# Optimization experiments

Measured on AMD Instinct MI355X. Metric: run time of the kernel, lower is better.

## Reference

```python
import jax, jax.numpy as jnp
import numpy as np

N = 200000      # active voxels
CIN = 96        # in_channels == out_channels (identity residual path)
CMID = 192      # max(in,out) * channel_multiplier
OFF = 27        # kernel_size**3 offsets
EPS = 1e-5      # BatchNorm eps


def setup_inputs() -> dict:
    key = jax.random.key(0)
    ks = jax.random.split(key, 6)
    x = jax.random.normal(ks[0], (N, CIN), jnp.float32)
    idx = jax.random.randint(ks[1], (OFF, N), 0, N, jnp.int32)
    mask = jax.random.randint(ks[2], (OFF, N), 0, 2, jnp.int32)
    W1 = jax.random.normal(ks[3], (OFF, CIN, CMID), jnp.float32) / np.float32(np.sqrt(OFF * CIN))
    W2 = jax.random.normal(ks[4], (OFF, CMID, CIN), jnp.float32) / np.float32(np.sqrt(OFF * CMID))
    g1 = jnp.ones((CMID,), jnp.float32)
    b1 = jnp.zeros((CMID,), jnp.float32)
    g2 = jnp.ones((CIN,), jnp.float32)
    b2 = jnp.zeros((CIN,), jnp.float32)
    return {"x": x, "idx": idx, "mask": mask, "W1": W1, "g1": g1, "b1": b1,
            "W2": W2, "g2": g2, "b2": b2}


def _sparse_conv(x, idx, mask, W):
    """Explicit-GEMM sparse conv: per-offset gather -> GEMM -> accumulate.
    x: [N, Cin], idx/mask: [OFF, N], W: [OFF, Cin, Cout] -> [N, Cout]."""
    n = x.shape[0]
    cout = W.shape[-1]

    def body(acc, off):
        i, m, w = off
        g = jnp.where(m[:, None] > 0, x[i], jnp.zeros((), x.dtype))  # gather [N, Cin]
        return acc + g @ w, None

    out, _ = jax.lax.scan(body, jnp.zeros((n, cout), x.dtype), (idx, mask, W))
    return out


def _bn(x, gamma, beta):
    # BatchNorm1d in training mode: batch statistics over the voxel dim.
    mu = jnp.mean(x, axis=0)
    var = jnp.var(x, axis=0)
    return gamma * (x - mu) * jax.lax.rsqrt(var + EPS) + beta


def reference(x, idx, mask, W1, g1, b1, W2, g2, b2):
    h = jax.nn.relu(_bn(_sparse_conv(x, idx, mask, W1), g1, b1))
    h = _bn(_sparse_conv(h, idx, mask, W2), g2, b2)
    return jax.nn.relu(h + x)  # identity residual (in_channels == out_channels)
```

## Files before the change

### kernel.cpp

```cpp
#include <hip/hip_runtime.h>
#include <hip/hip_bf16.h>

typedef unsigned short u16;
typedef __attribute__((ext_vector_type(8))) short short8;
typedef __attribute__((ext_vector_type(4))) float f32x4;
typedef __attribute__((ext_vector_type(8))) unsigned short ushort8v;

#define NVOX 200000
#define NVP  200064
#define NOFF 27
#define NBLK 1563

__device__ __forceinline__ u16 f2bf(float f) {
    __hip_bfloat16 h = __float2bfloat16(f);
    return *reinterpret_cast<u16*>(&h);
}
__device__ __forceinline__ float bf2f(u16 u) {
    union { unsigned int i; float f; } v;
    v.i = ((unsigned int)u) << 16;
    return v.f;
}

#define GLOAD_LDS16(g, l)                                                     \
    __builtin_amdgcn_global_load_lds(                                         \
        (const __attribute__((address_space(1))) unsigned int*)(g),           \
        (__attribute__((address_space(3))) unsigned int*)(l), 16, 0, 0)

__device__ __forceinline__ uint4 gld128(const u16* p) {
    uint4 r;
    asm volatile("global_load_dwordx4 %0, %1, off" : "=v"(r) : "v"(p) : "memory");
    return r;
}
__device__ __forceinline__ int gld32(const int* p) {
    int r;
    asm volatile("global_load_dword %0, %1, off" : "=v"(r) : "v"(p) : "memory");
    return r;
}
__device__ __forceinline__ uint4 dsr128(const u16* p) {
    uint4 r;
    asm volatile("ds_read_b128 %0, %1"
                 : "=v"(r)
                 : "v"((const __attribute__((address_space(3))) uint4*)p));
    return r;
}
__device__ __forceinline__ short8 as_s8(uint4 v) {
    union { uint4 u; short8 s; } c; c.u = v; return c.s;
}
#define S_WAIT_VM(n) asm volatile("s_waitcnt vmcnt(" #n ")" ::: "memory")
#define S_WAIT_LG(n) asm volatile("s_waitcnt lgkmcnt(" #n ")" ::: "memory")
#define SBAR0()      __builtin_amdgcn_sched_barrier(0)

__global__ __launch_bounds__(256) void prep_kernel(
    const float* __restrict__ x, const float* __restrict__ W1,
    const float* __restrict__ W2, u16* __restrict__ xb,
    u16* __restrict__ w1t, u16* __restrict__ w2t, float* __restrict__ zbuf)
{
    const int XV = NVOX * 96 / 4;
    const int WC = 62208;
    int t = blockIdx.x * 256 + threadIdx.x;
    if (blockIdx.x == 0 && threadIdx.x < 64) zbuf[threadIdx.x] = 0.f;
    if (t < XV) {
        float4 v = *(const float4*)(x + (size_t)t * 4);
        ushort4 o;
        o.x = f2bf(v.x); o.y = f2bf(v.y); o.z = f2bf(v.z); o.w = f2bf(v.w);
        *(ushort4*)(xb + (size_t)t * 4) = o;
    } else if (t < XV + WC) {
        int j = t - XV;
        int lane = j & 63, rest = j >> 6;
        int nco = rest % 12, rest2 = rest / 12;
        int ks = rest2 % 3, off = rest2 / 3;
        int co = nco * 16 + (lane & 15);
        int kb = ks * 32 + (lane >> 4) * 8;
        const float* src = W1 + (size_t)off * 18432 + (size_t)kb * 192 + co;
        ushort8v ov;
#pragma unroll
        for (int jj = 0; jj < 8; ++jj) ov[jj] = f2bf(src[(size_t)jj * 192]);
        *(ushort8v*)(w1t + (size_t)j * 8) = ov;
    } else if (t < XV + 2 * WC) {
        int j = t - XV - WC;
        int lane = j & 63, rest = j >> 6;
        int nco = rest % 6, rest2 = rest / 6;
        int kk = rest2 % 6, off = rest2 / 6;
        int co = nco * 16 + (lane & 15);
        int kb = kk * 32 + (lane >> 4) * 8;
        const float* src = W2 + (size_t)off * 18432 + (size_t)kb * 96 + co;
        ushort8v ov;
#pragma unroll
        for (int jj = 0; jj < 8; ++jj) ov[jj] = f2bf(src[(size_t)jj * 96]);
        *(ushort8v*)(w2t + (size_t)j * 8) = ov;
    }
}

__global__ __launch_bounds__(256) void lsrc_kernel(
    const int* __restrict__ idxp, const int* __restrict__ mskp,
    int* __restrict__ lsrcG)
{
    int r = blockIdx.x * 256 + threadIdx.x;
    int o = blockIdx.y;
    if (r < NVP) {
        int v = -1;
        if (r < NVOX) {
            if (mskp[(size_t)o * NVOX + r] > 0) v = idxp[(size_t)o * NVOX + r];
        }
        lsrcG[(size_t)o * NVP + r] = v;
    }
}

template<int COUT, int WN, int HFDIV>
__global__ __launch_bounds__(512, 4) void conv_mfma(
    const u16* __restrict__ xb, const int* __restrict__ lsrcG,
    const u16* __restrict__ Wt, const float* __restrict__ zbuf,
    u16* __restrict__ hout, float* __restrict__ part)
{
    constexpr int CIN  = 96 * HFDIV;
    constexpr int WM   = 8 / WN;
    constexpr int FM   = 128 / (WM * 16);
    constexpr int FN   = COUT / (WN * 16);
    constexpr int NCO  = COUT / 16;
    constexpr int SG   = NOFF * HFDIV;
    constexpr int BUFU = 12288;
    constexpr int WSTP = 3 * NCO * 512;

    __shared__ u16 ldsA[3 * BUFU];

    const int tid  = threadIdx.x;
    const int row0 = blockIdx.x * 128;
    const int lane = tid & 63;
    const int wid  = tid >> 6;
    const int wm   = wid / WN;
    const int wn   = wid % WN;
    const int lr   = lane & 15;
    const int lk   = lane >> 4;

    const int rStage = wid * 16 + (lane & 15);
    const int cBase  = (lane >> 4) * 8;
    const int ldsWaveBase = wid * 512;

    int rdBase[FM];
#pragma unroll
    for (int m = 0; m < FM; ++m)
        rdBase[m] = (wm * FM + m) * 512 + lr * 8 + lk * 128;
    const u16* wtw = Wt + (size_t)(wn * FN) * 512 + (size_t)lane * 8;
    const int* lsp = lsrcG + row0 + rStage;

    f32x4 acc[FM][FN];
#pragma unroll
    for (int m = 0; m < FM; ++m)
#pragma unroll
        for (int n = 0; n < FN; ++n)
            acc[m][n] = (f32x4){0.f, 0.f, 0.f, 0.f};

    auto gatherTo = [&](int sv, int hf, int bsel) {
        const u16* g = (sv >= 0)
            ? (xb + (size_t)sv * CIN + hf * 96 + cBase)
            : ((const u16*)zbuf + cBase);
#pragma unroll
        for (int it = 0; it < 3; ++it)
            GLOAD_LDS16(g + it * 32,
                        ldsA + bsel * BUFU + it * 4096 + ldsWaveBase);
    };
    auto svAddr = [&](int s) -> const int* {
        int idx2 = (s < SG) ? s : (SG - 1);
        int offIdx = (HFDIV == 1) ? idx2 : (idx2 >> 1);
        return lsp + (size_t)offIdx * NVP;
    };

    uint4 wregU[3 * FN];
    auto loadW = [&](const u16* wb) {
#pragma unroll
        for (int ks = 0; ks < 3; ++ks)
#pragma unroll
            for (int n = 0; n < FN; ++n)
                wregU[ks * FN + n] = gld128(wb + (ks * NCO + n) * 512);
    };
    auto mfmaPhase = [&](int cur) {
        const u16* abuf = ldsA + cur * BUFU;
        uint4 a[FM], b[FM];
#pragma unroll
        for (int m = 0; m < FM; ++m) a[m] = dsr128(abuf + rdBase[m]);
#pragma unroll
        for (int m = 0; m < FM; ++m) b[m] = dsr128(abuf + 4096 + rdBase[m]);
        if constexpr (FM == 4) S_WAIT_LG(4); else S_WAIT_LG(2);
        SBAR0();
#pragma unroll
        for (int m = 0; m < FM; ++m)
#pragma unroll
            for (int n = 0; n < FN; ++n)
                acc[m][n] = __builtin_amdgcn_mfma_f32_16x16x32_bf16(
                    as_s8(a[m]), as_s8(wregU[n]), acc[m][n], 0, 0, 0);
#pragma unroll
        for (int m = 0; m < FM; ++m) a[m] = dsr128(abuf + 8192 + rdBase[m]);
        if constexpr (FM == 4) S_WAIT_LG(4); else S_WAIT_LG(2);
        SBAR0();
#pragma unroll
        for (int m = 0; m < FM; ++m)
#pragma unroll
            for (int n = 0; n < FN; ++n)
                acc[m][n] = __builtin_amdgcn_mfma_f32_16x16x32_bf16(
                    as_s8(b[m]), as_s8(wregU[FN + n]), acc[m][n], 0, 0, 0);
        S_WAIT_LG(0);
        SBAR0();
#pragma unroll
        for (int m = 0; m < FM; ++m)
#pragma unroll
            for (int n = 0; n < FN; ++n)
                acc[m][n] = __builtin_amdgcn_mfma_f32_16x16x32_bf16(
                    as_s8(a[m]), as_s8(wregU[2 * FN + n]), acc[m][n], 0, 0, 0);
    };

    int sv0 = gld32(svAddr(0));
    int sv1 = gld32(svAddr(1));
    S_WAIT_VM(0); SBAR0();
    gatherTo(sv0, 0, 0);
    gatherTo(sv1, (HFDIV == 1) ? 0 : 1, 1);
    int svPend = gld32(svAddr(2));
    S_WAIT_VM(4); SBAR0();
    __builtin_amdgcn_s_barrier();
    SBAR0();

    const u16* wb = wtw;
    int cur = 0, nxt2 = 2;
#pragma unroll 1
    for (int s = 0; s < SG - 2; ++s) {
        loadW(wb);  wb += WSTP;
        SBAR0();
        S_WAIT_VM(9); SBAR0();
        int sv = svPend;
        gatherTo(sv, (HFDIV == 1) ? 0 : ((s + 2) & 1), nxt2);
        svPend = gld32(svAddr(s + 3));
        SBAR0();
        S_WAIT_VM(4); SBAR0();
        mfmaPhase(cur);
        SBAR0();
        __builtin_amdgcn_s_barrier();
        SBAR0();
        cur  = (cur == 2)  ? 0 : cur + 1;
        nxt2 = (nxt2 == 2) ? 0 : nxt2 + 1;
    }
    loadW(wb);  wb += WSTP;
    SBAR0();
    S_WAIT_VM(0); SBAR0();
    mfmaPhase(cur);
    SBAR0();
    __builtin_amdgcn_s_barrier();
    SBAR0();
    cur = (cur == 2) ? 0 : cur + 1;
    loadW(wb);
    SBAR0();
    S_WAIT_VM(0); SBAR0();
    mfmaPhase(cur);

    __syncthreads();
    float* smf = (float*)ldsA;
#pragma unroll
    for (int n = 0; n < FN; ++n) {
        float s1 = 0.f, s2 = 0.f;
#pragma unroll
        for (int m = 0; m < FM; ++m)
#pragma unroll
            for (int q = 0; q < 4; ++q) {
                float v = acc[m][n][q];
                s1 += v; s2 += v * v;
            }
        s1 += __shfl_xor(s1, 16); s1 += __shfl_xor(s1, 32);
        s2 += __shfl_xor(s2, 16); s2 += __shfl_xor(s2, 32);
        if (lane < 16) {
            int col = wn * (FN * 16) + n * 16 + lr;
            smf[(wm * COUT + col) * 2 + 0] = s1;
            smf[(wm * COUT + col) * 2 + 1] = s2;
        }
    }
    __syncthreads();
    if (tid < 2 * COUT) {
        int z = tid / COUT, cc = tid % COUT;
        float v = 0.f;
#pragma unroll
        for (int w = 0; w < WM; ++w) v += smf[(w * COUT + cc) * 2 + z];
        part[(size_t)blockIdx.x * (2 * COUT) + z * COUT + cc] = v;
    }

#pragma unroll
    for (int m = 0; m < FM; ++m) {
#pragma unroll
        for (int q = 0; q < 4; ++q) {
            int row = row0 + wm * (FM * 16) + m * 16 + lk * 4 + q;
            if (row < NVOX) {
#pragma unroll
                for (int n = 0; n < FN; ++n) {
                    int col = wn * (FN * 16) + n * 16 + lr;
                    hout[(size_t)row * COUT + col] = f2bf(acc[m][n][q]);
                }
            }
        }
    }
}

template<int COUT>
__global__ __launch_bounds__(256) void bn_statsB(
    const float* __restrict__ part, const float* __restrict__ g,
    const float* __restrict__ bv, float* __restrict__ ss)
{
    const int c = blockIdx.x;
    const int t = threadIdx.x;
    float s1 = 0.f, s2 = 0.f;
    for (int b = t; b < NBLK; b += 256) {
        s1 += part[(size_t)b * 2 * COUT + c];
        s2 += part[(size_t)b * 2 * COUT + COUT + c];
    }
#pragma unroll
    for (int d = 1; d < 64; d <<= 1) {
        s1 += __shfl_xor(s1, d);
        s2 += __shfl_xor(s2, d);
    }
    __shared__ float rs[8];
    int w = t >> 6;
    if ((t & 63) == 0) { rs[w] = s1; rs[4 + w] = s2; }
    __syncthreads();
    if (t == 0) {
        s1 = rs[0] + rs[1] + rs[2] + rs[3];
        s2 = rs[4] + rs[5] + rs[6] + rs[7];
        float mu  = s1 * (1.0f / NVOX);
        float var = s2 * (1.0f / NVOX) - mu * mu;
        float sc  = g[c] * rsqrtf(var + 1e-5f);
        ss[c] = sc;
        ss[COUT + c] = bv[c] - mu * sc;
    }
}

template<int COUT>
__global__ __launch_bounds__(256) void bn_apply_relu(
    u16* __restrict__ h, const float* __restrict__ ss)
{
    int t = blockIdx.x * 256 + threadIdx.x;
    int c0 = (t * 8) % COUT;
    ushort8v v = *(ushort8v*)(h + (size_t)t * 8);
#pragma unroll
    for (int j = 0; j < 8; ++j) {
        float f = bf2f(v[j]);
        f = fmaxf(f * ss[c0 + j] + ss[COUT + c0 + j], 0.f);
        v[j] = f2bf(f);
    }
    *(ushort8v*)(h + (size_t)t * 8) = v;
}

__global__ __launch_bounds__(256) void final_kernel(
    const u16* __restrict__ h2, const float* __restrict__ x,
    const float* __restrict__ ss, float* __restrict__ out)
{
    int t = blockIdx.x * 256 + threadIdx.x;
    int c0 = (t * 8) % 96;
    ushort8v v = *(const ushort8v*)(h2 + (size_t)t * 8);
    float4 x0 = *(const float4*)(x + (size_t)t * 8);
    float4 x1 = *(const float4*)(x + (size_t)t * 8 + 4);
    float xs[8] = {x0.x, x0.y, x0.z, x0.w, x1.x, x1.y, x1.z, x1.w};
    float o[8];
#pragma unroll
    for (int j = 0; j < 8; ++j) {
        float f = bf2f(v[j]) * ss[c0 + j] + ss[96 + c0 + j] + xs[j];
        o[j] = fmaxf(f, 0.f);
    }
    *(float4*)(out + (size_t)t * 8)     = (float4){o[0], o[1], o[2], o[3]};
    *(float4*)(out + (size_t)t * 8 + 4) = (float4){o[4], o[5], o[6], o[7]};
}

extern "C" void kernel_launch(void* const* d_in, const int* in_sizes, int n_in,
                              void* d_out, int out_size, void* d_ws, size_t ws_size,
                              hipStream_t stream)
{
    const float* x    = (const float*)d_in[0];
    const int*   idx  = (const int*)d_in[1];
    const int*   mask = (const int*)d_in[2];
    const float* W1   = (const float*)d_in[3];
    const float* g1   = (const float*)d_in[4];
    const float* b1   = (const float*)d_in[5];
    const float* W2   = (const float*)d_in[6];
    const float* g2   = (const float*)d_in[7];
    const float* b2   = (const float*)d_in[8];

    unsigned char* ws = (unsigned char*)d_ws;
    u16*  xb    = (u16*)ws;
    u16*  w1t   = (u16*)(ws + 38400000);
    u16*  w2t   = (u16*)(ws + 39395328);
    u16*  h2    = (u16*)(ws + 40390656);
    float* part = (float*)(ws + 78790656);
    float* ss1  = (float*)(ws + 81191424);
    float* ss2  = (float*)(ws + 81192960);
    float* zbuf = (float*)(ws + 81193728);
    int*  lsrcG = (int*)(ws + 81193984);

    u16* h = (u16*)d_out;

    prep_kernel<<<19236, 256, 0, stream>>>(x, W1, W2, xb, w1t, w2t, zbuf);
    lsrc_kernel<<<dim3(782, 27), 256, 0, stream>>>(idx, mask, lsrcG);

    conv_mfma<192, 4, 1><<<NBLK, 512, 0, stream>>>(xb, lsrcG, w1t, zbuf, h, part);
    bn_statsB<192><<<192, 256, 0, stream>>>(part, g1, b1, ss1);
    bn_apply_relu<192><<<18750, 256, 0, stream>>>(h, ss1);

    conv_mfma<96, 2, 2><<<NBLK, 512, 0, stream>>>(h, lsrcG, w2t, zbuf, h2, part);
    bn_statsB<96><<<96, 256, 0, stream>>>(part, g2, b2, ss2);
    final_kernel<<<9375, 256, 0, stream>>>(h2, x, ss2, (float*)d_out);
}
```

Measured before the change: 703.5 us.

## Stage conv weights into double-buffered LDS via direct global-to-LDS loads

Each wave no longer loads its weight fragments from global memory into registers. The block now cooperatively stages each offset's weight slice into a double-buffered LDS region using global_load_lds, with the weights repacked and padded in prep so the copies are contiguous. MFMA phases then read weights with ds_read alongside the activation reads. The aim is to cut redundant global weight traffic, since every wave re-read the same slice, and to lower VGPR pressure. In exchange LDS use grows and launch bounds drop from 4 to 2 blocks per CU, which may reduce occupancy.

```diff
diff --git a/kernel.cpp b/kernel.cpp
--- a/kernel.cpp
+++ b/kernel.cpp
@@ -26,11 +26,6 @@
         (const __attribute__((address_space(1))) unsigned int*)(g),           \
         (__attribute__((address_space(3))) unsigned int*)(l), 16, 0, 0)
 
-__device__ __forceinline__ uint4 gld128(const u16* p) {
-    uint4 r;
-    asm volatile("global_load_dwordx4 %0, %1, off" : "=v"(r) : "v"(p) : "memory");
-    return r;
-}
 __device__ __forceinline__ int gld32(const int* p) {
     int r;
     asm volatile("global_load_dword %0, %1, off" : "=v"(r) : "v"(p) : "memory");
@@ -75,19 +70,21 @@
         ushort8v ov;
 #pragma unroll
         for (int jj = 0; jj < 8; ++jj) ov[jj] = f2bf(src[(size_t)jj * 192]);
-        *(ushort8v*)(w1t + (size_t)j * 8) = ov;
+        *(ushort8v*)(w1t + (size_t)off * 20480 + (ks * 12 + nco) * 512 + lane * 8) = ov;
     } else if (t < XV + 2 * WC) {
         int j = t - XV - WC;
         int lane = j & 63, rest = j >> 6;
         int nco = rest % 6, rest2 = rest / 6;
-        int kk = rest2 % 6, off = rest2 / 6;
+        int ks = rest2 % 3, rest3 = rest2 / 3;
+        int hf = rest3 % 2, off = rest3 / 2;
         int co = nco * 16 + (lane & 15);
-        int kb = kk * 32 + (lane >> 4) * 8;
+        int kb = hf * 96 + ks * 32 + (lane >> 4) * 8;
         const float* src = W2 + (size_t)off * 18432 + (size_t)kb * 96 + co;
         ushort8v ov;
 #pragma unroll
         for (int jj = 0; jj < 8; ++jj) ov[jj] = f2bf(src[(size_t)jj * 96]);
-        *(ushort8v*)(w2t + (size_t)j * 8) = ov;
+        *(ushort8v*)(w2t + (size_t)(off * 2 + hf) * 12288 +
+                     (ks * 6 + nco) * 512 + lane * 8) = ov;
     }
 }
 
@@ -107,7 +104,7 @@
 }
 
 template<int COUT, int WN, int HFDIV>
-__global__ __launch_bounds__(512, 4) void conv_mfma(
+__global__ __launch_bounds__(512, 2) void conv_mfma(
     const u16* __restrict__ xb, const int* __restrict__ lsrcG,
     const u16* __restrict__ Wt, const float* __restrict__ zbuf,
     u16* __restrict__ hout, float* __restrict__ part)
@@ -119,9 +116,12 @@
     constexpr int NCO  = COUT / 16;
     constexpr int SG   = NOFF * HFDIV;
     constexpr int BUFU = 12288;
-    constexpr int WSTP = 3 * NCO * 512;
+    constexpr int WPAD = (COUT == 192) ? 2560 : 1536;
+    constexpr int WCH  = WPAD / 512;
+    constexpr int WBUFU = WPAD * 8;
 
     __shared__ u16 ldsA[3 * BUFU];
+    __shared__ u16 ldsW[2 * WBUFU];
 
     const int tid  = threadIdx.x;
     const int row0 = blockIdx.x * 128;
@@ -135,12 +135,13 @@
     const int rStage = wid * 16 + (lane & 15);
     const int cBase  = (lane >> 4) * 8;
     const int ldsWaveBase = wid * 512;
+    const int wStageBase  = (tid & ~63) * 8;
 
     int rdBase[FM];
 #pragma unroll
     for (int m = 0; m < FM; ++m)
         rdBase[m] = (wm * FM + m) * 512 + lr * 8 + lk * 128;
-    const u16* wtw = Wt + (size_t)(wn * FN) * 512 + (size_t)lane * 8;
+    const int wfBase = (wn * FN) * 512 + lane * 8;
     const int* lsp = lsrcG + row0 + rStage;
 
     f32x4 acc[FM][FN];
@@ -150,54 +151,60 @@
         for (int n = 0; n < FN; ++n)
             acc[m][n] = (f32x4){0.f, 0.f, 0.f, 0.f};
 
-    auto gatherTo = [&](int sv, int hf, int bsel) {
-        const u16* g = (sv >= 0)
-            ? (xb + (size_t)sv * CIN + hf * 96 + cBase)
-            : ((const u16*)zbuf + cBase);
-#pragma unroll
-        for (int it = 0; it < 3; ++it)
-            GLOAD_LDS16(g + it * 32,
-                        ldsA + bsel * BUFU + it * 4096 + ldsWaveBase);
-    };
+    auto hfOf = [&](int s) -> int { return (HFDIV == 1) ? 0 : (s & 1); };
     auto svAddr = [&](int s) -> const int* {
         int idx2 = (s < SG) ? s : (SG - 1);
         int offIdx = (HFDIV == 1) ? idx2 : (idx2 >> 1);
         return lsp + (size_t)offIdx * NVP;
     };
-
-    uint4 wregU[3 * FN];
-    auto loadW = [&](const u16* wb) {
-#pragma unroll
-        for (int ks = 0; ks < 3; ++ks)
-#pragma unroll
-            for (int n = 0; n < FN; ++n)
-                wregU[ks * FN + n] = gld128(wb + (ks * NCO + n) * 512);
+    auto gatherTo = [&](int sv, int hf, int bsel) {
+        const u16* g = (sv >= 0)
+            ? (xb + (size_t)sv * CIN + hf * 96 + cBase)
+            : ((const u16*)zbuf + cBase);
+#pragma unroll
+        for (int it = 0; it < 3; ++it)
+            GLOAD_LDS16(g + it * 32,
+                        ldsA + bsel * BUFU + it * 4096 + ldsWaveBase);
     };
-    auto mfmaPhase = [&](int cur) {
+    auto stageW = [&](int s, int wsel) {
+        const u16* src = Wt + (size_t)s * WBUFU + (size_t)tid * 8;
+        u16* dst = ldsW + wsel * WBUFU + wStageBase;
+#pragma unroll
+        for (int it = 0; it < WCH; ++it)
+            GLOAD_LDS16(src + it * 4096, dst + it * 4096);
+    };
+    auto mfmaPhase = [&](int cur, int wsel) {
         const u16* abuf = ldsA + cur * BUFU;
-        uint4 a[FM], b[FM];
-#pragma unroll
-        for (int m = 0; m < FM; ++m) a[m] = dsr128(abuf + rdBase[m]);
-#pragma unroll
-        for (int m = 0; m < FM; ++m) b[m] = dsr128(abuf + 4096 + rdBase[m]);
-        if constexpr (FM == 4) S_WAIT_LG(4); else S_WAIT_LG(2);
+        const u16* wbuf = ldsW + wsel * WBUFU + wfBase;
+        uint4 a0[FM], a1[FM], w0[FN], w1[FN];
+#pragma unroll
+        for (int n = 0; n < FN; ++n) w0[n] = dsr128(wbuf + n * 512);
+#pragma unroll
+        for (int m = 0; m < FM; ++m) a0[m] = dsr128(abuf + rdBase[m]);
+#pragma unroll
+        for (int n = 0; n < FN; ++n) w1[n] = dsr128(wbuf + (NCO + n) * 512);
+#pragma unroll
+        for (int m = 0; m < FM; ++m) a1[m] = dsr128(abuf + 4096 + rdBase[m]);
+        if constexpr (FM == 4) S_WAIT_LG(7); else S_WAIT_LG(5);
         SBAR0();
 #pragma unroll
         for (int m = 0; m < FM; ++m)
 #pragma unroll
             for (int n = 0; n < FN; ++n)
                 acc[m][n] = __builtin_amdgcn_mfma_f32_16x16x32_bf16(
-                    as_s8(a[m]), as_s8(wregU[n]), acc[m][n], 0, 0, 0);
-#pragma unroll
-        for (int m = 0; m < FM; ++m) a[m] = dsr128(abuf + 8192 + rdBase[m]);
-        if constexpr (FM == 4) S_WAIT_LG(4); else S_WAIT_LG(2);
+                    as_s8(a0[m]), as_s8(w0[n]), acc[m][n], 0, 0, 0);
+#pragma unroll
+        for (int n = 0; n < FN; ++n) w0[n] = dsr128(wbuf + (2 * NCO + n) * 512);
+#pragma unroll
+        for (int m = 0; m < FM; ++m) a0[m] = dsr128(abuf + 8192 + rdBase[m]);
+        if constexpr (FM == 4) S_WAIT_LG(7); else S_WAIT_LG(5);
         SBAR0();
 #pragma unroll
         for (int m = 0; m < FM; ++m)
 #pragma unroll
             for (int n = 0; n < FN; ++n)
                 acc[m][n] = __builtin_amdgcn_mfma_f32_16x16x32_bf16(
-                    as_s8(b[m]), as_s8(wregU[FN + n]), acc[m][n], 0, 0, 0);
+                    as_s8(a1[m]), as_s8(w1[n]), acc[m][n], 0, 0, 0);
         S_WAIT_LG(0);
         SBAR0();
 #pragma unroll
@@ -205,50 +212,49 @@
 #pragma unroll
             for (int n = 0; n < FN; ++n)
                 acc[m][n] = __builtin_amdgcn_mfma_f32_16x16x32_bf16(
-                    as_s8(a[m]), as_s8(wregU[2 * FN + n]), acc[m][n], 0, 0, 0);
+                    as_s8(a0[m]), as_s8(w0[n]), acc[m][n], 0, 0, 0);
     };
 
-    int sv0 = gld32(svAddr(0));
-    int sv1 = gld32(svAddr(1));
-    S_WAIT_VM(0); SBAR0();
-    gatherTo(sv0, 0, 0);
-    gatherTo(sv1, (HFDIV == 1) ? 0 : 1, 1);
-    int svPend = gld32(svAddr(2));
-    S_WAIT_VM(4); SBAR0();
-    __builtin_amdgcn_s_barrier();
-    SBAR0();
-
-    const u16* wb = wtw;
+    int svC;
+    {
+        int sv0 = gld32(svAddr(0));
+        int sv1 = gld32(svAddr(1));
+        int sv2 = gld32(svAddr(2));
+        S_WAIT_VM(0); SBAR0();
+        stageW(0, 0);
+        gatherTo(sv0, hfOf(0), 0);
+        gatherTo(sv1, hfOf(1), 1);
+        svC = sv2;
+        S_WAIT_VM(3); SBAR0();
+        __builtin_amdgcn_s_barrier();
+        SBAR0();
+    }
+
     int cur = 0, nxt2 = 2;
 #pragma unroll 1
     for (int s = 0; s < SG - 2; ++s) {
-        loadW(wb);  wb += WSTP;
-        SBAR0();
-        S_WAIT_VM(9); SBAR0();
-        int sv = svPend;
-        gatherTo(sv, (HFDIV == 1) ? 0 : ((s + 2) & 1), nxt2);
-        svPend = gld32(svAddr(s + 3));
-        SBAR0();
-        S_WAIT_VM(4); SBAR0();
-        mfmaPhase(cur);
+        stageW(s + 1, (s + 1) & 1);
+        int svN = gld32(svAddr(s + 3));
+        gatherTo(svC, hfOf(s + 2), nxt2);
+        SBAR0();
+        S_WAIT_VM(3); SBAR0();
+        mfmaPhase(cur, s & 1);
         SBAR0();
         __builtin_amdgcn_s_barrier();
         SBAR0();
+        svC = svN;
         cur  = (cur == 2)  ? 0 : cur + 1;
         nxt2 = (nxt2 == 2) ? 0 : nxt2 + 1;
     }
-    loadW(wb);  wb += WSTP;
+    stageW(SG - 1, (SG - 1) & 1);
     SBAR0();
     S_WAIT_VM(0); SBAR0();
-    mfmaPhase(cur);
+    mfmaPhase(cur, (SG - 2) & 1);
     SBAR0();
     __builtin_amdgcn_s_barrier();
     SBAR0();
     cur = (cur == 2) ? 0 : cur + 1;
-    loadW(wb);
-    SBAR0();
-    S_WAIT_VM(0); SBAR0();
-    mfmaPhase(cur);
+    mfmaPhase(cur, (SG - 1) & 1);
 
     __syncthreads();
     float* smf = (float*)ldsA;
@@ -380,13 +386,13 @@
     unsigned char* ws = (unsigned char*)d_ws;
     u16*  xb    = (u16*)ws;
     u16*  w1t   = (u16*)(ws + 38400000);
-    u16*  w2t   = (u16*)(ws + 39395328);
-    u16*  h2    = (u16*)(ws + 40390656);
-    float* part = (float*)(ws + 78790656);
-    float* ss1  = (float*)(ws + 81191424);
-    float* ss2  = (float*)(ws + 81192960);
-    float* zbuf = (float*)(ws + 81193728);
-    int*  lsrcG = (int*)(ws + 81193984);
+    u16*  w2t   = (u16*)(ws + 39505920);
+    u16*  h2    = (u16*)(ws + 40833024);
+    float* part = (float*)(ws + 79233024);
+    float* ss1  = (float*)(ws + 81633792);
+    float* ss2  = (float*)(ws + 81635328);
+    float* zbuf = (float*)(ws + 81636096);
+    int*  lsrcG = (int*)(ws + 81636352);
 
     u16* h = (u16*)d_out;
 
```

New measurement: 740.2 us. +5.2%, slower.
